# Kernel tuning notes

Hardware: AMD Instinct MI355X
Metric: run time of the kernel (lower is better)

Reference implementation:

```python
import jax, jax.numpy as jnp
import numpy as np

INPUT_SIZE = 1024
ATTN_SIZE = 1024


def setup_inputs() -> dict:
    key = jax.random.key(0)
    ks = jax.random.split(key, 7)
    s = 1.0 / np.sqrt(INPUT_SIZE)
    x = jax.random.normal(ks[0], (2048, 8, INPUT_SIZE), dtype=jnp.float32)
    Wq = jax.random.uniform(ks[1], (ATTN_SIZE, INPUT_SIZE), jnp.float32, -s, s)
    bq = jax.random.uniform(ks[2], (ATTN_SIZE,), jnp.float32, -s, s)
    Wk = jax.random.uniform(ks[3], (ATTN_SIZE, INPUT_SIZE), jnp.float32, -s, s)
    bk = jax.random.uniform(ks[4], (ATTN_SIZE,), jnp.float32, -s, s)
    Wv = jax.random.uniform(ks[5], (ATTN_SIZE, INPUT_SIZE), jnp.float32, -s, s)
    bv = jax.random.uniform(ks[6], (ATTN_SIZE,), jnp.float32, -s, s)
    return {"x": x, "Wq": Wq, "bq": bq, "Wk": Wk, "bk": bk, "Wv": Wv, "bv": bv}


def reference(x, Wq, bq, Wk, bk, Wv, bv):
    # x: (S, B, D) -> (B, S, D)
    xb = jnp.swapaxes(x, 0, 1)
    Q = jnp.einsum('bsd,ad->bsa', xb, Wq) + bq  # (B, S, A)
    K = jnp.einsum('bsd,ad->bsa', xb, Wk) + bk
    V = jnp.einsum('bsd,ad->bsa', xb, Wv) + bv
    S = Q.shape[1]
    scores = jnp.einsum('bqa,bka->bqk', Q, K) / jnp.sqrt(jnp.float32(ATTN_SIZE))
    causal = jnp.tril(jnp.ones((S, S), dtype=bool))  # True where attended
    scores = jnp.where(causal, scores, -jnp.inf)
    probs = jax.nn.softmax(scores, axis=-1)
    out = jnp.einsum('bqk,bka->bqa', probs, V)  # (B, S, A)
    return jnp.swapaxes(out, 0, 1)  # (S, B, A)
```

## Files before the change

### kernel.cpp

```cpp
#include <hip/hip_runtime.h>
#include <hip/hip_bf16.h>
#include <math.h>

typedef short bf16x8 __attribute__((ext_vector_type(8)));
typedef float f32x4 __attribute__((ext_vector_type(4)));
typedef short short4v __attribute__((ext_vector_type(4)));
typedef short short8v __attribute__((ext_vector_type(8)));

__device__ __forceinline__ short f2bf(float f) {
  unsigned u = __builtin_bit_cast(unsigned, f);
  unsigned r = (u + 0x7FFFu + ((u >> 16) & 1u)) >> 16;
  return (short)r;
}
__device__ __forceinline__ float bf2f(short s) {
  unsigned u = ((unsigned)(unsigned short)s) << 16;
  return __builtin_bit_cast(float, u);
}

typedef __attribute__((address_space(1))) const unsigned g_u32;
typedef __attribute__((address_space(3))) unsigned l_u32;
__device__ __forceinline__ void gload_lds16(const short* g, short* l) {
  __builtin_amdgcn_global_load_lds((g_u32*)g, (l_u32*)l, 16, 0, 0);
}

#define VMCNT(n) asm volatile("s_waitcnt vmcnt(" #n ")" ::: "memory")


__global__ __launch_bounds__(256) void k_cast_x(const float* __restrict__ x, short* __restrict__ xb) {
  int tid = blockIdx.x * 256 + threadIdx.x;
  int d4 = tid & 255;
  int sb = tid >> 8;
  int s = sb & 2047;
  int b = sb >> 11;
  float4 v = *((const float4*)(x + (((size_t)s * 8 + b) << 10)) + d4);
  short4v o;
  o.x = f2bf(v.x); o.y = f2bf(v.y); o.z = f2bf(v.z); o.w = f2bf(v.w);
  *((short4v*)(xb + (((size_t)b * 2048 + s) << 10)) + d4) = o;
}

__global__ __launch_bounds__(256) void k_cast_w(const float* __restrict__ Wq, const float* __restrict__ Wk,
                                                const float* __restrict__ Wv, short* __restrict__ Wcat) {
  int tid = blockIdx.x * 256 + threadIdx.x;
  int d4 = tid & 255;
  int n = tid >> 8;
  const float* src = (n < 1024) ? Wq : (n < 2048 ? Wk : Wv);
  int nl = n & 1023;
  float4 v = *((const float4*)(src + ((size_t)nl << 10)) + d4);
  short4v o;
  o.x = f2bf(v.x); o.y = f2bf(v.y); o.z = f2bf(v.z); o.w = f2bf(v.w);
  *((short4v*)(Wcat + ((size_t)n << 10)) + d4) = o;
}

__global__ __launch_bounds__(256) void k_cast_bias(const float* __restrict__ bq, const float* __restrict__ bk,
                                                   const float* __restrict__ bv, float* __restrict__ biascat) {
  int i = blockIdx.x * 256 + threadIdx.x;
  if (i < 3072) biascat[i] = (i < 1024) ? bq[i] : (i < 2048 ? bk[i & 1023] : bv[i & 1023]);
}

template <int LDA, int LDB>
__device__ __forceinline__ void gemm256_core(const short* __restrict__ Ag, const short* __restrict__ Bg,
                                             int NT, short* __restrict__ lds, f32x4 (&acc)[8][4], int tid) {
  const int lane = tid & 63;
  const int wid = tid >> 6;
  const int wm = wid >> 2, wn = wid & 3;
  const int r15 = lane & 15;
  const int g = lane >> 4;
  const int co = ((g ^ ((r15 >> 1) & 3)) << 3);
  short* As = lds;
  short* Bs = lds + 32768;

  const int abase = (wm * 128 + r15) * 32 + co;
  const int bbase = (wn * 64 + r15) * 32 + co;

  auto stageA = [&](int c) {
    short* Lp = As + ((c & 3) << 13);
    int kb = c << 5;
#pragma unroll
    for (int i = 0; i < 2; ++i) {
      int ch = i * 512 + tid;
      int r = ch >> 2, s = ch & 3;
      gload_lds16(Ag + (size_t)r * LDA + kb + ((s ^ ((r >> 1) & 3)) << 3), Lp + ch * 8);
    }
  };
  auto stageB = [&](int c) {
    short* Lp = Bs + ((c & 3) << 13);
    int kb = c << 5;
#pragma unroll
    for (int i = 0; i < 2; ++i) {
      int ch = i * 512 + tid;
      int r = ch >> 2, s = ch & 3;
      gload_lds16(Bg + (size_t)r * LDB + kb + ((s ^ ((r >> 1) & 3)) << 3), Lp + ch * 8);
    }
  };

  bf16x8 a4[4], br[4];
  auto rdA = [&](int c, int mh) {
    const short* p = As + ((c & 3) << 13) + abase + (mh << 11);
#pragma unroll
    for (int mf = 0; mf < 4; ++mf) a4[mf] = *(const bf16x8*)(p + mf * 512);
  };
  auto rdB = [&](int c) {
    const short* p = Bs + ((c & 3) << 13) + bbase;
#pragma unroll
    for (int nf = 0; nf < 4; ++nf) br[nf] = *(const bf16x8*)(p + nf * 512);
  };
  auto mm = [&](int mh) {
    __builtin_amdgcn_s_barrier();
    asm volatile("s_waitcnt lgkmcnt(0)" ::: "memory");
    __builtin_amdgcn_sched_barrier(0);
    __builtin_amdgcn_s_setprio(1);
#pragma unroll
    for (int mf = 0; mf < 4; ++mf)
#pragma unroll
      for (int nf = 0; nf < 4; ++nf)
        acc[mh * 4 + mf][nf] =
            __builtin_amdgcn_mfma_f32_16x16x32_bf16(a4[mf], br[nf], acc[mh * 4 + mf][nf], 0, 0, 0);
    __builtin_amdgcn_s_setprio(0);
    __builtin_amdgcn_s_barrier();
  };

  stageB(0); stageA(0); stageB(1); stageA(1); stageB(2); stageA(2); stageB(3);
  VMCNT(10);
  __builtin_amdgcn_s_barrier();

  for (int t = 0; t + 2 < NT; ++t) {
    const int c0 = 2 * t, c1 = 2 * t + 1;
    rdA(c0, 0); rdB(c0); stageA(c0 + 3);
    mm(0);
    rdA(c0, 1); stageB(c0 + 4); VMCNT(10);
    mm(1);
    rdA(c1, 0); rdB(c1); stageA(c1 + 3);
    mm(0);
    rdA(c1, 1); stageB(c1 + 4); VMCNT(10);
    mm(1);
  }
  {
    const int c0 = 2 * (NT - 2), c1 = c0 + 1;
    rdA(c0, 0); rdB(c0); stageA(c0 + 3);
    mm(0);
    rdA(c0, 1); VMCNT(8);
    mm(1);
    rdA(c1, 0); rdB(c1);
    mm(0);
    rdA(c1, 1); VMCNT(4);
    mm(1);
  }
  {
    const int c0 = 2 * (NT - 1), c1 = c0 + 1;
    rdA(c0, 0); rdB(c0);
    mm(0);
    rdA(c0, 1); VMCNT(0);
    mm(1);
    rdA(c1, 0); rdB(c1);
    mm(0);
    rdA(c1, 1);
    mm(1);
  }
}

__global__ __launch_bounds__(512, 1) void k_proj(const short* __restrict__ Xb, const short* __restrict__ Wc,
                                                 const float* __restrict__ biascat,
                                                 short* __restrict__ Q, short* __restrict__ K, short* __restrict__ Vt) {
  __shared__ __align__(16) short lds[65536];
  int tid = threadIdx.x;
  int wg = blockIdx.x;
  int swz = (wg & 7) * 96 + (wg >> 3);
  int mt = swz / 12, nt = swz % 12;
  int m0 = mt << 8, n0 = nt << 8;
  f32x4 acc[8][4] = {};
  gemm256_core<1024, 1024>(Xb + (size_t)m0 * 1024, Wc + (size_t)n0 * 1024, 16, lds, acc, tid);
  int lane = tid & 63, wid = tid >> 6;
  int wm = wid >> 2, wn = wid & 3;
  int r15 = lane & 15;
  int which = n0 >> 10;
  int nbase = n0 & 1023;
  if (which == 2) {
#pragma unroll
    for (int ni = 0; ni < 4; ++ni) {
      int cth = wn * 64 + ni * 16 + r15;
      int a = nbase + cth;
      float bv = biascat[n0 + cth];
#pragma unroll
      for (int mi = 0; mi < 8; ++mi) {
        int r = m0 + wm * 128 + mi * 16 + ((lane >> 4) << 2);
        int b = r >> 11, s = r & 2047;
        short4v o;
#pragma unroll
        for (int j = 0; j < 4; ++j) o[j] = f2bf(acc[mi][ni][j] + bv);
        *(short4v*)(Vt + ((size_t)b << 21) + ((size_t)a << 11) + s) = o;
      }
    }
  } else {
    short* outb = (which == 0) ? Q : K;
#pragma unroll
    for (int ni = 0; ni < 4; ++ni) {
      int cth = wn * 64 + ni * 16 + r15;
      float bv = biascat[n0 + cth];
#pragma unroll
      for (int mi = 0; mi < 8; ++mi)
#pragma unroll
        for (int j = 0; j < 4; ++j) {
          int r = m0 + wm * 128 + mi * 16 + ((lane >> 4) << 2) + j;
          outb[((size_t)r << 10) + nbase + cth] = f2bf(acc[mi][ni][j] + bv);
        }
    }
  }
}

__global__ __launch_bounds__(512, 1) void k_qk(const short* __restrict__ Q, const short* __restrict__ K,
                                               short* __restrict__ Sc) {
  int nt = blockIdx.x, mt = blockIdx.y, b = blockIdx.z;
  if (nt > mt) return;
  __shared__ __align__(16) short lds[65536];
  int tid = threadIdx.x;
  int m0 = mt << 8, n0 = nt << 8;
  const short* Qb = Q + ((size_t)b << 21);
  const short* Kb = K + ((size_t)b << 21);
  f32x4 acc[8][4] = {};
  gemm256_core<1024, 1024>(Qb + (size_t)m0 * 1024, Kb + (size_t)n0 * 1024, 16, lds, acc, tid);
  short* Sb = Sc + ((size_t)b << 22);
  int lane = tid & 63, wid = tid >> 6;
  int wm = wid >> 2, wn = wid & 3;
  int r15 = lane & 15;
#pragma unroll
  for (int mi = 0; mi < 8; ++mi)
#pragma unroll
    for (int ni = 0; ni < 4; ++ni)
#pragma unroll
      for (int j = 0; j < 4; ++j) {
        int r = m0 + wm * 128 + mi * 16 + ((lane >> 4) << 2) + j;
        int c = n0 + wn * 64 + ni * 16 + r15;
        Sb[((size_t)r << 11) + c] = f2bf(acc[mi][ni][j] * 0.03125f);
      }
}

__global__ __launch_bounds__(256) void k_softmax(short* __restrict__ Sc) {
  int row = blockIdx.x;
  int b = row >> 11, q = row & 2047;
  short* Pr = Sc + ((size_t)b << 22) + ((size_t)q << 11);
  int T = ((q >> 8) + 1) << 8;
  int tid = threadIdx.x, lane = tid & 63, wid = tid >> 6;
  int k0 = tid << 3;
  float v[8];
  if (k0 < T) {
    short8v raw = *(const short8v*)(Pr + k0);
#pragma unroll
    for (int j = 0; j < 8; ++j) v[j] = (k0 + j <= q) ? bf2f(raw[j]) : -__builtin_inff();
  } else {
#pragma unroll
    for (int j = 0; j < 8; ++j) v[j] = -__builtin_inff();
  }
  float mx = v[0];
#pragma unroll
  for (int j = 1; j < 8; ++j) mx = fmaxf(mx, v[j]);
  for (int off = 1; off < 64; off <<= 1) mx = fmaxf(mx, __shfl_xor(mx, off, 64));
  __shared__ float red[2][4];
  if (lane == 0) red[0][wid] = mx;
  __syncthreads();
  mx = fmaxf(fmaxf(red[0][0], red[0][1]), fmaxf(red[0][2], red[0][3]));
  float e[8], sum = 0.f;
#pragma unroll
  for (int j = 0; j < 8; ++j) {
    e[j] = exp2f((v[j] - mx) * 1.4426950408889634f);
    sum += e[j];
  }
  for (int off = 1; off < 64; off <<= 1) sum += __shfl_xor(sum, off, 64);
  if (lane == 0) red[1][wid] = sum;
  __syncthreads();
  sum = red[1][0] + red[1][1] + red[1][2] + red[1][3];
  float inv = 1.f / sum;
  if (k0 < T) {
    short8v o;
#pragma unroll
    for (int j = 0; j < 8; ++j) o[j] = (k0 + j <= q) ? f2bf(e[j] * inv) : (short)0;
    *(short8v*)(Pr + k0) = o;
  }
}

__global__ __launch_bounds__(512, 1) void k_pv(const short* __restrict__ P, const short* __restrict__ Vt,
                                               float* __restrict__ out) {
  int nt = blockIdx.x, mt = blockIdx.y, b = blockIdx.z;
  __shared__ __align__(16) short lds[65536];
  int tid = threadIdx.x;
  int m0 = mt << 8, n0 = nt << 8;
  const short* Pb = P + ((size_t)b << 22);
  const short* Vtb = Vt + ((size_t)b << 21);
  f32x4 acc[8][4] = {};
  gemm256_core<2048, 2048>(Pb + (size_t)m0 * 2048, Vtb + (size_t)n0 * 2048, 4 * (mt + 1), lds, acc, tid);
  int lane = tid & 63, wid = tid >> 6;
  int wm = wid >> 2, wn = wid & 3;
  int r15 = lane & 15;
#pragma unroll
  for (int mi = 0; mi < 8; ++mi)
#pragma unroll
    for (int ni = 0; ni < 4; ++ni)
#pragma unroll
      for (int j = 0; j < 4; ++j) {
        int r = m0 + wm * 128 + mi * 16 + ((lane >> 4) << 2) + j;
        int c = n0 + wn * 64 + ni * 16 + r15;
        out[((size_t)r << 13) + ((size_t)b << 10) + c] = acc[mi][ni][j];
      }
}

extern "C" void kernel_launch(void* const* d_in, const int* in_sizes, int n_in,
                              void* d_out, int out_size, void* d_ws, size_t ws_size,
                              hipStream_t stream) {
  const float* x  = (const float*)d_in[0];
  const float* Wq = (const float*)d_in[1];
  const float* bq = (const float*)d_in[2];
  const float* Wk = (const float*)d_in[3];
  const float* bk = (const float*)d_in[4];
  const float* Wv = (const float*)d_in[5];
  const float* bv = (const float*)d_in[6];
  float* out = (float*)d_out;
  char* ws = (char*)d_ws;

  short* xb   = (short*)(ws);
  short* Wcat = (short*)(ws + 33554432);
  float* bias = (float*)(ws + 39845888);
  short* Q    = (short*)(ws + 39858176);
  short* K    = (short*)(ws + 73412608);
  short* Vt   = (short*)(ws + 106967040);
  short* Sc   = (short*)(ws + 140521472);

  k_cast_x<<<16384, 256, 0, stream>>>(x, xb);
  k_cast_w<<<3072, 256, 0, stream>>>(Wq, Wk, Wv, Wcat);
  k_cast_bias<<<12, 256, 0, stream>>>(bq, bk, bv, bias);
  k_proj<<<768, 512, 0, stream>>>(xb, Wcat, bias, Q, K, Vt);
  k_qk<<<dim3(8, 8, 8), 512, 0, stream>>>(Q, K, Sc);
  k_softmax<<<16384, 256, 0, stream>>>(Sc);
  k_pv<<<dim3(4, 8, 8), 512, 0, stream>>>(Sc, Vt, out);
}
```

Baseline: 284.2 us.

## Use 256x128 tiles for projection GEMM and remap QK/PV grids with XCD swizzle

Adds a new 256x128 GEMM core with a triple-buffered LDS pipeline and BK=32 for the projection kernel. It halves the LDS footprint and raises launch bounds so more workgroups can be resident per CU, and doubles the grid to 1536 blocks. QK now launches only the lower-triangular tiles through a flattened, XCD-swizzled index, so no idle blocks exit early. PV also uses a swizzled flat grid. The cost is a smaller tile per block, which means less data reuse, and extra index arithmetic.

Result: faster. 273.9 us (-3.6%).

```diff
diff --git a/kernel.cpp b/kernel.cpp
--- a/kernel.cpp
+++ b/kernel.cpp
@@ -158,20 +158,88 @@
   }
 }
 
-__global__ __launch_bounds__(512, 1) void k_proj(const short* __restrict__ Xb, const short* __restrict__ Wc,
+template <int LDA, int LDB>
+__device__ __forceinline__ void gemm128n_core(const short* __restrict__ Ag, const short* __restrict__ Bg,
+                                              int NC, short* __restrict__ lds, f32x4 (&acc)[4][4], int tid) {
+  const int lane = tid & 63;
+  const int wid = tid >> 6;
+  const int wm = wid >> 1, wn = wid & 1;
+  const int r15 = lane & 15;
+  const int g = lane >> 4;
+  const int co = ((g ^ ((r15 >> 1) & 3)) << 3);
+  short* As = lds;
+  short* Bs = lds + 3 * 8192;
+
+  const int abase = (wm * 64 + r15) * 32 + co;
+  const int bbase = (wn * 64 + r15) * 32 + co;
+
+  auto stage_pair = [&](int c) {
+    short* Ap = As + (c % 3) * 8192;
+    short* Bp = Bs + (c % 3) * 4096;
+    int kb = c << 5;
+#pragma unroll
+    for (int i = 0; i < 2; ++i) {
+      int ch = i * 512 + tid;
+      int r = ch >> 2, s = ch & 3;
+      gload_lds16(Ag + (size_t)r * LDA + kb + ((s ^ ((r >> 1) & 3)) << 3), Ap + ch * 8);
+    }
+    {
+      int r = tid >> 2, s = tid & 3;
+      gload_lds16(Bg + (size_t)r * LDB + kb + ((s ^ ((r >> 1) & 3)) << 3), Bp + tid * 8);
+    }
+  };
+
+  auto phase = [&](int c, bool stage, bool last) {
+    bf16x8 a4[4], br[4];
+    const short* pa = As + (c % 3) * 8192 + abase;
+    const short* pb = Bs + (c % 3) * 4096 + bbase;
+#pragma unroll
+    for (int mf = 0; mf < 4; ++mf) a4[mf] = *(const bf16x8*)(pa + mf * 512);
+#pragma unroll
+    for (int nf = 0; nf < 4; ++nf) br[nf] = *(const bf16x8*)(pb + nf * 512);
+    if (stage) {
+      stage_pair(c + 2);
+      VMCNT(3);
+    } else if (!last) {
+      VMCNT(0);
+    }
+    __builtin_amdgcn_s_barrier();
+    asm volatile("s_waitcnt lgkmcnt(0)" ::: "memory");
+    __builtin_amdgcn_sched_barrier(0);
+    __builtin_amdgcn_s_setprio(1);
+#pragma unroll
+    for (int mf = 0; mf < 4; ++mf)
+#pragma unroll
+      for (int nf = 0; nf < 4; ++nf)
+        acc[mf][nf] = __builtin_amdgcn_mfma_f32_16x16x32_bf16(a4[mf], br[nf], acc[mf][nf], 0, 0, 0);
+    __builtin_amdgcn_s_setprio(0);
+    __builtin_amdgcn_s_barrier();
+  };
+
+  stage_pair(0);
+  stage_pair(1);
+  VMCNT(3);
+  __builtin_amdgcn_s_barrier();
+
+  for (int c = 0; c < NC - 2; ++c) phase(c, true, false);
+  phase(NC - 2, false, false);
+  phase(NC - 1, false, true);
+}
+
+__global__ __launch_bounds__(512, 4) void k_proj(const short* __restrict__ Xb, const short* __restrict__ Wc,
                                                  const float* __restrict__ biascat,
                                                  short* __restrict__ Q, short* __restrict__ K, short* __restrict__ Vt) {
-  __shared__ __align__(16) short lds[65536];
+  __shared__ __align__(16) short lds[36864];
   int tid = threadIdx.x;
   int wg = blockIdx.x;
-  int swz = (wg & 7) * 96 + (wg >> 3);
-  int mt = swz / 12, nt = swz % 12;
-  int m0 = mt << 8, n0 = nt << 8;
-  f32x4 acc[8][4] = {};
-  gemm256_core<1024, 1024>(Xb + (size_t)m0 * 1024, Wc + (size_t)n0 * 1024, 16, lds, acc, tid);
+  int swz = (wg & 7) * 192 + (wg >> 3);
+  int mt = swz / 24, nt = swz % 24;
+  int m0 = mt << 8, n0 = nt << 7;
+  f32x4 acc[4][4] = {};
+  gemm128n_core<1024, 1024>(Xb + (size_t)m0 * 1024, Wc + (size_t)n0 * 1024, 32, lds, acc, tid);
   int lane = tid & 63, wid = tid >> 6;
-  int wm = wid >> 2, wn = wid & 3;
-  int r15 = lane & 15;
+  int wm = wid >> 1, wn = wid & 1;
+  int r15 = lane & 15, g = lane >> 4;
   int which = n0 >> 10;
   int nbase = n0 & 1023;
   if (which == 2) {
@@ -181,8 +249,8 @@
       int a = nbase + cth;
       float bv = biascat[n0 + cth];
 #pragma unroll
-      for (int mi = 0; mi < 8; ++mi) {
-        int r = m0 + wm * 128 + mi * 16 + ((lane >> 4) << 2);
+      for (int mi = 0; mi < 4; ++mi) {
+        int r = m0 + wm * 64 + mi * 16 + g * 4;
         int b = r >> 11, s = r & 2047;
         short4v o;
 #pragma unroll
@@ -197,10 +265,10 @@
       int cth = wn * 64 + ni * 16 + r15;
       float bv = biascat[n0 + cth];
 #pragma unroll
-      for (int mi = 0; mi < 8; ++mi)
+      for (int mi = 0; mi < 4; ++mi)
 #pragma unroll
         for (int j = 0; j < 4; ++j) {
-          int r = m0 + wm * 128 + mi * 16 + ((lane >> 4) << 2) + j;
+          int r = m0 + wm * 64 + mi * 16 + g * 4 + j;
           outb[((size_t)r << 10) + nbase + cth] = f2bf(acc[mi][ni][j] + bv);
         }
     }
@@ -209,9 +277,15 @@
 
 __global__ __launch_bounds__(512, 1) void k_qk(const short* __restrict__ Q, const short* __restrict__ K,
                                                short* __restrict__ Sc) {
-  int nt = blockIdx.x, mt = blockIdx.y, b = blockIdx.z;
-  if (nt > mt) return;
   __shared__ __align__(16) short lds[65536];
+  int f = blockIdx.x;
+  int swz = (f & 7) * 36 + (f >> 3);
+  int b = swz / 36;
+  int t = swz % 36;
+  int mt = (int)((sqrtf(8.f * t + 1.f) - 1.f) * 0.5f);
+  while ((mt + 1) * (mt + 2) / 2 <= t) ++mt;
+  while (mt * (mt + 1) / 2 > t) --mt;
+  int nt = t - mt * (mt + 1) / 2;
   int tid = threadIdx.x;
   int m0 = mt << 8, n0 = nt << 8;
   const short* Qb = Q + ((size_t)b << 21);
@@ -279,8 +353,12 @@
 
 __global__ __launch_bounds__(512, 1) void k_pv(const short* __restrict__ P, const short* __restrict__ Vt,
                                                float* __restrict__ out) {
-  int nt = blockIdx.x, mt = blockIdx.y, b = blockIdx.z;
   __shared__ __align__(16) short lds[65536];
+  int f = blockIdx.x;
+  int swz = (f & 7) * 32 + (f >> 3);
+  int nt = swz & 3;
+  int mt = (swz >> 2) & 7;
+  int b = swz >> 5;
   int tid = threadIdx.x;
   int m0 = mt << 8, n0 = nt << 8;
   const short* Pb = P + ((size_t)b << 22);
@@ -326,8 +404,8 @@
   k_cast_x<<<16384, 256, 0, stream>>>(x, xb);
   k_cast_w<<<3072, 256, 0, stream>>>(Wq, Wk, Wv, Wcat);
   k_cast_bias<<<12, 256, 0, stream>>>(bq, bk, bv, bias);
-  k_proj<<<768, 512, 0, stream>>>(xb, Wcat, bias, Q, K, Vt);
-  k_qk<<<dim3(8, 8, 8), 512, 0, stream>>>(Q, K, Sc);
+  k_proj<<<1536, 512, 0, stream>>>(xb, Wcat, bias, Q, K, Vt);
+  k_qk<<<288, 512, 0, stream>>>(Q, K, Sc);
   k_softmax<<<16384, 256, 0, stream>>>(Sc);
-  k_pv<<<dim3(4, 8, 8), 512, 0, stream>>>(Sc, Vt, out);
-}
+  k_pv<<<256, 512, 0, stream>>>(Sc, Vt, out);
+}
```
